# Kernel tuning notes

Measured on AMD Instinct MI355X. Metric: run time of the kernel, lower is better.

The kernel has to match this reference:

```python
import jax, jax.numpy as jnp
import numpy as np

B, S, H = 1024, 512, 768
D1, D2 = 128, 1


def setup_inputs() -> dict:
    key = jax.random.key(0)
    k_feat, k_start, k_len, k_w1, k_w2 = jax.random.split(key, 5)
    features_extract = jax.random.normal(k_feat, (B, S, H), dtype=jnp.float32)
    start_token_idx = jax.random.randint(k_start, (B,), 1, 200, dtype=jnp.int64)
    span_len = jax.random.randint(k_len, (B,), 1, 65, dtype=jnp.int64)
    end_token_idx = start_token_idx + span_len  # guaranteed start < end <= 264 < S
    W1 = jax.random.normal(k_w1, (2 * H, D1), dtype=jnp.float32) * (1.0 / np.sqrt(2 * H))
    b1 = jnp.zeros((D1,), dtype=jnp.float32)
    W2 = jax.random.normal(k_w2, (D1, D2), dtype=jnp.float32) * (1.0 / np.sqrt(D1))
    b2 = jnp.zeros((D2,), dtype=jnp.float32)
    return {
        "features_extract": features_extract,
        "start_token_idx": start_token_idx,
        "end_token_idx": end_token_idx,
        "W1": W1, "b1": b1, "W2": W2, "b2": b2,
    }


def reference(features_extract, start_token_idx, end_token_idx, W1, b1, W2, b2):
    # CLS feature: token 0 of each example -> [B, 1, H]
    features_cls = features_extract[:, 0, :][:, None, :]

    # Ragged span mean-pool (vectorized replacement for the per-example loop):
    # mask[b, s] = start[b] <= s < end[b]
    pos = jnp.arange(features_extract.shape[1])  # [S]
    mask = (pos[None, :] >= start_token_idx[:, None]) & (pos[None, :] < end_token_idx[:, None])
    maskf = mask.astype(features_extract.dtype)  # [B, S]
    span_sum = jnp.einsum('bsh,bs->bh', features_extract, maskf)
    span_len = (end_token_idx - start_token_idx).astype(features_extract.dtype)  # >= 1
    features_crc = (span_sum / span_len[:, None])[:, None, :]  # [B, 1, H]

    # Concat + MLP head (dropout layers are identity in eval)
    features = jnp.concatenate([features_cls, features_crc], axis=2)  # [B, 1, 2H]
    h = jax.nn.relu(jnp.einsum('bid,dk->bik', features, W1) + b1)
    out = jax.nn.sigmoid(jnp.einsum('bik,ko->bio', h, W2) + b2)  # [B, 1, 1]
    return out
```

## Files before the change

kernel.cpp:

```cpp
#include <hip/hip_runtime.h>
#include <math.h>

constexpr int Bn = 1024;
constexpr int S  = 512;
constexpr int H  = 768;
constexpr int D1 = 128;
constexpr int HV = H / 4;
constexpr int K2 = 2 * H;
constexpr int NK = K2 / 32;
constexpr int NKH = NK / 2;
constexpr int NCAST = 16;

typedef _Float16 half8 __attribute__((ext_vector_type(8)));
typedef _Float16 half4v __attribute__((ext_vector_type(4)));
typedef float floatx4 __attribute__((ext_vector_type(4)));


__device__ __forceinline__ size_t swz_off(int tile, int kk, int lg, int idx) {
  return ((((size_t)tile * NK + kk) * 64) + lg * 16 + idx) * 8;
}

__global__ __launch_bounds__(256) void pool_cast(
    const float* __restrict__ feat, const int* __restrict__ start,
    const int* __restrict__ endp, const float* __restrict__ W1,
    _Float16* __restrict__ g16, _Float16* __restrict__ w1s) {
  __shared__ float4 pacc[4][3][64];
  const int t = threadIdx.x;

  if (blockIdx.x < NCAST) {
    const int c  = blockIdx.x;
    const int n  = t & 127;
    const int sb = t >> 7;
    const int nt = n >> 4, ni = n & 15;
    #pragma unroll
    for (int j = 0; j < 6; ++j) {
      const int k0 = c * 96 + sb * 48 + j * 8;
      _Float16 h[8];
      #pragma unroll
      for (int i = 0; i < 8; ++i) {
        h[i] = (_Float16)W1[(size_t)(k0 + i) * D1 + n];
      }
      const int kk = k0 >> 5, lg = (k0 >> 3) & 3;
      *reinterpret_cast<half8*>(w1s + swz_off(nt, kk, lg, ni)) =
          *reinterpret_cast<half8*>(h);
    }
    return;
  }

  const int b = blockIdx.x - NCAST;
  const int w = t >> 6;
  const int l = t & 63;
  const float4* base =
      reinterpret_cast<const float4*>(feat) + (size_t)b * (S * HV);

  if (t < 192) {
    float4 cv = base[t];
    half4v hc;
    hc.x = (_Float16)cv.x; hc.y = (_Float16)cv.y;
    hc.z = (_Float16)cv.z; hc.w = (_Float16)cv.w;
    *reinterpret_cast<half4v*>(g16 + (size_t)b * K2 + t * 4) = hc;
  }

  const int s0 = start[b];
  const int s1 = endp[b];

  float4 c0{0,0,0,0}, c1{0,0,0,0}, c2{0,0,0,0};
  float4 d0{0,0,0,0}, d1{0,0,0,0}, d2{0,0,0,0};
  int s = s0 + w;
  for (; s + 4 < s1; s += 8) {
    const float4* r0 = base + (size_t)s * HV;
    const float4* r1 = base + (size_t)(s + 4) * HV;
    float4 u0 = r0[l], u1 = r0[l + 64], u2 = r0[l + 128];
    float4 v0 = r1[l], v1 = r1[l + 64], v2 = r1[l + 128];
    c0.x += u0.x; c0.y += u0.y; c0.z += u0.z; c0.w += u0.w;
    c1.x += u1.x; c1.y += u1.y; c1.z += u1.z; c1.w += u1.w;
    c2.x += u2.x; c2.y += u2.y; c2.z += u2.z; c2.w += u2.w;
    d0.x += v0.x; d0.y += v0.y; d0.z += v0.z; d0.w += v0.w;
    d1.x += v1.x; d1.y += v1.y; d1.z += v1.z; d1.w += v1.w;
    d2.x += v2.x; d2.y += v2.y; d2.z += v2.z; d2.w += v2.w;
  }
  for (; s < s1; s += 4) {
    const float4* r0 = base + (size_t)s * HV;
    float4 u0 = r0[l], u1 = r0[l + 64], u2 = r0[l + 128];
    c0.x += u0.x; c0.y += u0.y; c0.z += u0.z; c0.w += u0.w;
    c1.x += u1.x; c1.y += u1.y; c1.z += u1.z; c1.w += u1.w;
    c2.x += u2.x; c2.y += u2.y; c2.z += u2.z; c2.w += u2.w;
  }
  c0.x += d0.x; c0.y += d0.y; c0.z += d0.z; c0.w += d0.w;
  c1.x += d1.x; c1.y += d1.y; c1.z += d1.z; c1.w += d1.w;
  c2.x += d2.x; c2.y += d2.y; c2.z += d2.z; c2.w += d2.w;
  pacc[w][0][l] = c0;
  pacc[w][1][l] = c1;
  pacc[w][2][l] = c2;
  __syncthreads();

  if (t < 192) {
    const int seg = t >> 6, ln = t & 63;
    float4 a = pacc[0][seg][ln], bb = pacc[1][seg][ln];
    float4 cq = pacc[2][seg][ln], dq = pacc[3][seg][ln];
    const float inv = 1.0f / (float)(s1 - s0);
    half4v r;
    r.x = (_Float16)(((a.x + bb.x) + (cq.x + dq.x)) * inv);
    r.y = (_Float16)(((a.y + bb.y) + (cq.y + dq.y)) * inv);
    r.z = (_Float16)(((a.z + bb.z) + (cq.z + dq.z)) * inv);
    r.w = (_Float16)(((a.w + bb.w) + (cq.w + dq.w)) * inv);
    *reinterpret_cast<half4v*>(g16 + (size_t)b * K2 + H + t * 4) = r;
  }
}

__global__ __launch_bounds__(64) void head_mfma(
    const _Float16* __restrict__ g16, const _Float16* __restrict__ w1s,
    float* __restrict__ p0, float* __restrict__ p1) {
  const int l  = threadIdx.x;
  const int eg = blockIdx.x & 63;
  const int rest = blockIdx.x >> 6;
  const int nt = rest >> 1;
  const int kh = rest & 1;

  const int lg = l >> 4, li = l & 15;
  const int e0 = eg * 16;

  const _Float16* Abase = g16 + (size_t)(e0 + li) * K2 + kh * (K2 / 2) + lg * 8;
  const half8* Bp = reinterpret_cast<const half8*>(w1s) +
                    ((size_t)nt * NK + kh * NKH) * 64 + l;

  floatx4 acc0 = {0.f, 0.f, 0.f, 0.f};
  floatx4 acc1 = {0.f, 0.f, 0.f, 0.f};
  #pragma unroll 2
  for (int kk = 0; kk < NKH; kk += 4) {
    half8 a0 = *reinterpret_cast<const half8*>(Abase + (kk + 0) * 32);
    half8 b0 = Bp[(size_t)(kk + 0) * 64];
    half8 a1 = *reinterpret_cast<const half8*>(Abase + (kk + 1) * 32);
    half8 b1v = Bp[(size_t)(kk + 1) * 64];
    half8 a2 = *reinterpret_cast<const half8*>(Abase + (kk + 2) * 32);
    half8 b2v = Bp[(size_t)(kk + 2) * 64];
    half8 a3 = *reinterpret_cast<const half8*>(Abase + (kk + 3) * 32);
    half8 b3v = Bp[(size_t)(kk + 3) * 64];
    acc0 = __builtin_amdgcn_mfma_f32_16x16x32_f16(a0, b0, acc0, 0, 0, 0);
    acc1 = __builtin_amdgcn_mfma_f32_16x16x32_f16(a1, b1v, acc1, 0, 0, 0);
    acc0 = __builtin_amdgcn_mfma_f32_16x16x32_f16(a2, b2v, acc0, 0, 0, 0);
    acc1 = __builtin_amdgcn_mfma_f32_16x16x32_f16(a3, b3v, acc1, 0, 0, 0);
  }

  float* plane = kh ? p1 : p0;
  const int n = nt * 16 + li;
  #pragma unroll
  for (int r = 0; r < 4; ++r) {
    const int m = lg * 4 + r;
    plane[(size_t)(e0 + m) * D1 + n] = acc0[r] + acc1[r];
  }
}

__global__ __launch_bounds__(256) void fin(
    const float* __restrict__ p0, const float* __restrict__ p1,
    const float* __restrict__ b1, const float* __restrict__ W2,
    const float* __restrict__ b2, float* __restrict__ out) {
  const int t = threadIdx.x;
  const int w = t >> 6, l = t & 63;
  const int e = blockIdx.x * 4 + w;
  const int k0 = l, k1 = l + 64;
  const size_t base = (size_t)e * D1;
  float h0 = b1[k0] + p0[base + k0] + p1[base + k0];
  float h1 = b1[k1] + p0[base + k1] + p1[base + k1];
  h0 = fmaxf(h0, 0.f); h1 = fmaxf(h1, 0.f);
  float v = h0 * W2[k0] + h1 * W2[k1];
  #pragma unroll
  for (int off = 32; off > 0; off >>= 1) v += __shfl_down(v, off);
  if (l == 0) out[e] = 1.0f / (1.0f + expf(-(v + b2[0])));
}

extern "C" void kernel_launch(void* const* d_in, const int* in_sizes, int n_in,
                              void* d_out, int out_size, void* d_ws, size_t ws_size,
                              hipStream_t stream) {
  const float* feat = (const float*)d_in[0];
  const int* start  = (const int*)d_in[1];
  const int* endp   = (const int*)d_in[2];
  const float* W1   = (const float*)d_in[3];
  const float* b1   = (const float*)d_in[4];
  const float* W2   = (const float*)d_in[5];
  const float* b2   = (const float*)d_in[6];
  float* out = (float*)d_out;

  _Float16* g16 = (_Float16*)d_ws;
  _Float16* w1s = g16 + (size_t)Bn * K2;
  float* p0     = (float*)(w1s + (size_t)D1 * K2);
  float* p1     = p0 + (size_t)Bn * D1;

  hipLaunchKernelGGL(pool_cast, dim3(NCAST + Bn), dim3(256), 0, stream,
                     feat, start, endp, W1, g16, w1s);
  hipLaunchKernelGGL(head_mfma, dim3(1024), dim3(64), 0, stream,
                     g16, w1s, p0, p1);
  hipLaunchKernelGGL(fin, dim3(Bn / 4), dim3(256), 0, stream,
                     p0, p1, b1, W2, b2, out);
}
```

Measured before the change: 31.94 us.

## Compute CLS half of first layer inside pool kernel, split span GEMM

The CLS-token half of the first linear layer now runs as extra MFMA blocks inside the pooling launch. These blocks read fp32 features and W1 directly and convert them to fp16 in registers, so the CLS rows are no longer staged in fp16 and W1 rows for that half are no longer pre-swizzled. The second kernel handles only the span-mean half, split into two K-quarters that write separate partial planes, and the final kernel sums three partials. This cuts staging work and shrinks the second GEMM, but the fused CLS blocks make strided uncoalesced W1 loads and add another partial buffer to read.

```diff
diff --git a/kernel.cpp b/kernel.cpp
--- a/kernel.cpp
+++ b/kernel.cpp
@@ -8,8 +8,9 @@
 constexpr int HV = H / 4;
 constexpr int K2 = 2 * H;
 constexpr int NK = K2 / 32;
-constexpr int NKH = NK / 2;
-constexpr int NCAST = 16;
+constexpr int NKH = 24;
+constexpr int NCAST = 8;
+constexpr int NCLS = 128;
 
 typedef _Float16 half8 __attribute__((ext_vector_type(8)));
 typedef _Float16 half4v __attribute__((ext_vector_type(4)));
@@ -20,15 +21,16 @@
   return ((((size_t)tile * NK + kk) * 64) + lg * 16 + idx) * 8;
 }
 
-__global__ __launch_bounds__(256) void pool_cast(
+__global__ __launch_bounds__(256) void launch1(
     const float* __restrict__ feat, const int* __restrict__ start,
     const int* __restrict__ endp, const float* __restrict__ W1,
-    _Float16* __restrict__ g16, _Float16* __restrict__ w1s) {
+    _Float16* __restrict__ gcrc, _Float16* __restrict__ w1s,
+    float* __restrict__ p0) {
   __shared__ float4 pacc[4][3][64];
   const int t = threadIdx.x;
 
   if (blockIdx.x < NCAST) {
-    const int c  = blockIdx.x;
+    const int c  = blockIdx.x + 8;
     const int n  = t & 127;
     const int sb = t >> 7;
     const int nt = n >> 4, ni = n & 15;
@@ -47,19 +49,58 @@
     return;
   }
 
-  const int b = blockIdx.x - NCAST;
+  if (blockIdx.x < NCAST + NCLS) {
+    const int w = t >> 6, l = t & 63;
+    const int tid = (blockIdx.x - NCAST) * 4 + w;
+    const int eg = tid & 63;
+    const int nt = tid >> 6;
+    const int lg = l >> 4, li = l & 15;
+    const int e0 = eg * 16;
+    const int n = nt * 16 + li;
+
+    const float* arow = feat + (size_t)(e0 + li) * S * H;
+    const float* wcol = W1 + n;
+
+    floatx4 acc0 = {0.f, 0.f, 0.f, 0.f};
+    floatx4 acc1 = {0.f, 0.f, 0.f, 0.f};
+    #pragma unroll 2
+    for (int kk = 0; kk < NKH; kk += 2) {
+      #define MKFRAG(kkq, accq)                                            \
+      {                                                                    \
+        const int kb = (kkq) * 32 + lg * 8;                                \
+        float4 fa = *reinterpret_cast<const float4*>(arow + kb);           \
+        float4 fb = *reinterpret_cast<const float4*>(arow + kb + 4);       \
+        const float* wb = wcol + (size_t)kb * D1;                          \
+        float w0 = wb[0 * D1], w1v = wb[1 * D1], w2v = wb[2 * D1];         \
+        float w3v = wb[3 * D1], w4v = wb[4 * D1], w5v = wb[5 * D1];        \
+        float w6v = wb[6 * D1], w7v = wb[7 * D1];                          \
+        half8 av, bv;                                                      \
+        av[0] = (_Float16)fa.x; av[1] = (_Float16)fa.y;                    \
+        av[2] = (_Float16)fa.z; av[3] = (_Float16)fa.w;                    \
+        av[4] = (_Float16)fb.x; av[5] = (_Float16)fb.y;                    \
+        av[6] = (_Float16)fb.z; av[7] = (_Float16)fb.w;                    \
+        bv[0] = (_Float16)w0;  bv[1] = (_Float16)w1v;                      \
+        bv[2] = (_Float16)w2v; bv[3] = (_Float16)w3v;                      \
+        bv[4] = (_Float16)w4v; bv[5] = (_Float16)w5v;                      \
+        bv[6] = (_Float16)w6v; bv[7] = (_Float16)w7v;                      \
+        accq = __builtin_amdgcn_mfma_f32_16x16x32_f16(av, bv, accq, 0, 0, 0); \
+      }
+      MKFRAG(kk, acc0)
+      MKFRAG(kk + 1, acc1)
+      #undef MKFRAG
+    }
+    #pragma unroll
+    for (int r = 0; r < 4; ++r) {
+      p0[(size_t)(e0 + lg * 4 + r) * D1 + n] = acc0[r] + acc1[r];
+    }
+    return;
+  }
+
+  const int b = blockIdx.x - (NCAST + NCLS);
   const int w = t >> 6;
   const int l = t & 63;
   const float4* base =
       reinterpret_cast<const float4*>(feat) + (size_t)b * (S * HV);
-
-  if (t < 192) {
-    float4 cv = base[t];
-    half4v hc;
-    hc.x = (_Float16)cv.x; hc.y = (_Float16)cv.y;
-    hc.z = (_Float16)cv.z; hc.w = (_Float16)cv.w;
-    *reinterpret_cast<half4v*>(g16 + (size_t)b * K2 + t * 4) = hc;
-  }
 
   const int s0 = start[b];
   const int s1 = endp[b];
@@ -104,30 +145,30 @@
     r.y = (_Float16)(((a.y + bb.y) + (cq.y + dq.y)) * inv);
     r.z = (_Float16)(((a.z + bb.z) + (cq.z + dq.z)) * inv);
     r.w = (_Float16)(((a.w + bb.w) + (cq.w + dq.w)) * inv);
-    *reinterpret_cast<half4v*>(g16 + (size_t)b * K2 + H + t * 4) = r;
-  }
-}
-
-__global__ __launch_bounds__(64) void head_mfma(
-    const _Float16* __restrict__ g16, const _Float16* __restrict__ w1s,
-    float* __restrict__ p0, float* __restrict__ p1) {
+    *reinterpret_cast<half4v*>(gcrc + (size_t)b * H + t * 4) = r;
+  }
+}
+
+__global__ __launch_bounds__(64) void crc_mfma(
+    const _Float16* __restrict__ gcrc, const _Float16* __restrict__ w1s,
+    float* __restrict__ p1, float* __restrict__ p2) {
   const int l  = threadIdx.x;
   const int eg = blockIdx.x & 63;
   const int rest = blockIdx.x >> 6;
   const int nt = rest >> 1;
-  const int kh = rest & 1;
+  const int kq = rest & 1;
 
   const int lg = l >> 4, li = l & 15;
   const int e0 = eg * 16;
 
-  const _Float16* Abase = g16 + (size_t)(e0 + li) * K2 + kh * (K2 / 2) + lg * 8;
+  const _Float16* Abase = gcrc + (size_t)(e0 + li) * H + kq * 384 + lg * 8;
   const half8* Bp = reinterpret_cast<const half8*>(w1s) +
-                    ((size_t)nt * NK + kh * NKH) * 64 + l;
+                    ((size_t)nt * NK + NKH + kq * 12) * 64 + l;
 
   floatx4 acc0 = {0.f, 0.f, 0.f, 0.f};
   floatx4 acc1 = {0.f, 0.f, 0.f, 0.f};
-  #pragma unroll 2
-  for (int kk = 0; kk < NKH; kk += 4) {
+  #pragma unroll 3
+  for (int kk = 0; kk < 12; kk += 4) {
     half8 a0 = *reinterpret_cast<const half8*>(Abase + (kk + 0) * 32);
     half8 b0 = Bp[(size_t)(kk + 0) * 64];
     half8 a1 = *reinterpret_cast<const half8*>(Abase + (kk + 1) * 32);
@@ -142,26 +183,26 @@
     acc1 = __builtin_amdgcn_mfma_f32_16x16x32_f16(a3, b3v, acc1, 0, 0, 0);
   }
 
-  float* plane = kh ? p1 : p0;
+  float* plane = kq ? p2 : p1;
   const int n = nt * 16 + li;
   #pragma unroll
   for (int r = 0; r < 4; ++r) {
-    const int m = lg * 4 + r;
-    plane[(size_t)(e0 + m) * D1 + n] = acc0[r] + acc1[r];
+    plane[(size_t)(e0 + lg * 4 + r) * D1 + n] = acc0[r] + acc1[r];
   }
 }
 
 __global__ __launch_bounds__(256) void fin(
     const float* __restrict__ p0, const float* __restrict__ p1,
-    const float* __restrict__ b1, const float* __restrict__ W2,
-    const float* __restrict__ b2, float* __restrict__ out) {
+    const float* __restrict__ p2, const float* __restrict__ b1,
+    const float* __restrict__ W2, const float* __restrict__ b2,
+    float* __restrict__ out) {
   const int t = threadIdx.x;
   const int w = t >> 6, l = t & 63;
   const int e = blockIdx.x * 4 + w;
   const int k0 = l, k1 = l + 64;
   const size_t base = (size_t)e * D1;
-  float h0 = b1[k0] + p0[base + k0] + p1[base + k0];
-  float h1 = b1[k1] + p0[base + k1] + p1[base + k1];
+  float h0 = b1[k0] + p0[base + k0] + p1[base + k0] + p2[base + k0];
+  float h1 = b1[k1] + p0[base + k1] + p1[base + k1] + p2[base + k1];
   h0 = fmaxf(h0, 0.f); h1 = fmaxf(h1, 0.f);
   float v = h0 * W2[k0] + h1 * W2[k1];
   #pragma unroll
@@ -181,15 +222,16 @@
   const float* b2   = (const float*)d_in[6];
   float* out = (float*)d_out;
 
-  _Float16* g16 = (_Float16*)d_ws;
-  _Float16* w1s = g16 + (size_t)Bn * K2;
-  float* p0     = (float*)(w1s + (size_t)D1 * K2);
-  float* p1     = p0 + (size_t)Bn * D1;
-
-  hipLaunchKernelGGL(pool_cast, dim3(NCAST + Bn), dim3(256), 0, stream,
-                     feat, start, endp, W1, g16, w1s);
-  hipLaunchKernelGGL(head_mfma, dim3(1024), dim3(64), 0, stream,
-                     g16, w1s, p0, p1);
+  _Float16* gcrc = (_Float16*)d_ws;
+  _Float16* w1s  = gcrc + (size_t)Bn * H;
+  float* p0 = (float*)(w1s + (size_t)D1 * K2);
+  float* p1 = p0 + (size_t)Bn * D1;
+  float* p2 = p1 + (size_t)Bn * D1;
+
+  hipLaunchKernelGGL(launch1, dim3(NCAST + NCLS + Bn), dim3(256), 0, stream,
+                     feat, start, endp, W1, gcrc, w1s, p0);
+  hipLaunchKernelGGL(crc_mfma, dim3(1024), dim3(64), 0, stream,
+                     gcrc, w1s, p1, p2);
   hipLaunchKernelGGL(fin, dim3(Bn / 4), dim3(256), 0, stream,
-                     p0, p1, b1, W2, b2, out);
-}
+                     p0, p1, p2, b1, W2, b2, out);
+}
```

After: 30.59 us (median of 2 runs). 4.2% less time.
